# Optimization experiments

Measured on AMD Instinct MI355X. Metric: run time of the kernel, lower is better.

## Reference

```python
import jax, jax.numpy as jnp
import numpy as np

jax.config.update("jax_enable_x64", True)  # torch uses int64 labels with wrapping arithmetic

N = 100_000   # nodes
E = 3_200_000 # edges
D = 128       # label classes (argmax dim)
NUM_ITERATIONS = 3


def setup_inputs() -> dict:
    key = jax.random.key(0)
    k1, k2 = jax.random.split(key)
    x = jax.random.normal(k1, (N, D), dtype=jnp.float32)
    edge_index = jax.random.randint(k2, (2, E), 0, N, dtype=jnp.int64)
    return {"x": x, "edge_index": edge_index}


def _edge_exponents(row):
    """For each edge e, number of edges AFTER e (in edge order) sharing the same row.

    The torch loop computes neighborhood[r] = neighborhood[r]*31 + labels[c]
    sequentially over edges, i.e. for a row-group with targets c_1..c_k (edge order)
    the result is sum_j labels[c_j] * 31**(k - j). The exponent (k - j) is exactly
    the count of later same-row edges.
    """
    e = row.shape[0]
    order = jnp.argsort(row, stable=True)          # stable sort preserves edge order within groups
    srow = row[order]
    first = jnp.searchsorted(srow, srow, side="left")   # group start index
    last = jnp.searchsorted(srow, srow, side="right")   # group end index (exclusive)
    pos = jnp.arange(e) - first                          # position within group
    exp_sorted = (last - first) - 1 - pos                # edges remaining after this one
    return jnp.zeros(e, dtype=jnp.int64).at[order].set(exp_sorted)


def reference(x, edge_index):
    labels = jnp.argmax(x, axis=-1).astype(jnp.int64) if x.ndim > 1 else x.astype(jnp.int64)
    row, col = edge_index[0], edge_index[1]
    exps = _edge_exponents(row)
    # 31**exp in wrapping int64 arithmetic; exponentiation-by-squaring mod 2^64
    # matches the sequential multiply-add mod 2^64 of the torch loop.
    pow31 = jnp.power(jnp.int64(31), exps)
    history = [labels]
    for _ in range(NUM_ITERATIONS):
        vals = labels[col] * pow31                       # [E] per-edge weighted labels
        labels = jax.ops.segment_sum(vals, row, num_segments=N)  # ordered hash accumulate
        history.append(labels)
    return (labels, *history)
```

## Files before the change

### kernel.cpp

```cpp
#include <hip/hip_runtime.h>
#include <hip/hip_bf16.h>


#define WL_D 128
#define NCH 512
#define GRID_F 2048
#define BT 512
#define MSDW 8
#define BBITS 7
#define BROWS 128
#define NBK 1024
#define RLSHIFT 23
#define COLMASK ((1u << RLSHIFT) - 1u)
#define CMAX 5120
#define NBMAX 13
#define KBMAX 10
#define HP8 2487512833u

__device__ inline int xcd_chunk(int bid) { return ((bid & 7) << 6) | (bid >> 3); }

template <int BITS>
__device__ inline unsigned long long match_key(unsigned v) {
    unsigned long long m = ~0ull;
    #pragma unroll
    for (int b = 0; b < BITS; ++b) {
        unsigned long long s = __ballot((v >> b) & 1u);
        m &= ((v >> b) & 1u) ? s : ~s;
    }
    return m;
}

__global__ void __launch_bounds__(BT)
k_hist_argmax(const float* __restrict__ x, const int* __restrict__ ei,
              unsigned* __restrict__ lab0, unsigned* __restrict__ hist,
              int N, int E, int chunk, int nbuckets) {
    __shared__ unsigned h[NBK];
    int bid = blockIdx.x, t = threadIdx.x, lane = t & 63, w = t >> 6;
    if (bid < NCH) {
        int b = xcd_chunk(bid);
        for (int i = t; i < nbuckets; i += BT) h[i] = 0u;
        __syncthreads();
        int base = b * chunk, lim = min(base + chunk, E);
        int vbeg = (base + 3) & ~3; if (vbeg > lim) vbeg = lim;
        int vend = lim & ~3;        if (vend < vbeg) vend = vbeg;
        for (int e = base + t; e < vbeg; e += BT)
            atomicAdd(&h[((unsigned)ei[e]) >> BBITS], 1u);
        for (int i = vbeg + 4 * t; i < vend; i += 4 * BT) {
            int4 v4 = *(const int4*)(ei + i);
            atomicAdd(&h[((unsigned)v4.x) >> BBITS], 1u);
            atomicAdd(&h[((unsigned)v4.y) >> BBITS], 1u);
            atomicAdd(&h[((unsigned)v4.z) >> BBITS], 1u);
            atomicAdd(&h[((unsigned)v4.w) >> BBITS], 1u);
        }
        for (int e = vend + t; e < lim; e += BT)
            atomicAdd(&h[((unsigned)ei[e]) >> BBITS], 1u);
        __syncthreads();
        for (int v = t; v < nbuckets; v += BT) hist[(size_t)v * NCH + b] = h[v];
    } else {
        int ab = bid - NCH;
        int half = lane >> 5, li = lane & 31;
        for (int pr = ab * MSDW + w; 2 * pr < N; pr += (GRID_F - NCH) * MSDW) {
            int r = 2 * pr + half;
            float bv = -3.4e38f; int bi = 0;
            if (r < N) {
                float4 v = ((const float4*)(x + (size_t)r * WL_D))[li];
                bv = v.x; bi = 4 * li;
                if (v.y > bv) { bv = v.y; bi = 4 * li + 1; }
                if (v.z > bv) { bv = v.z; bi = 4 * li + 2; }
                if (v.w > bv) { bv = v.w; bi = 4 * li + 3; }
            }
            #pragma unroll
            for (int off = 16; off > 0; off >>= 1) {
                float ov = __shfl_down(bv, off, 32);
                int   oi = __shfl_down(bi, off, 32);
                if (ov > bv || (ov == bv && oi < bi)) { bv = ov; bi = oi; }
            }
            if (li == 0 && r < N) lab0[r] = (unsigned)bi;
        }
    }
}

__global__ void __launch_bounds__(BT)
k_scan_tile(unsigned* __restrict__ hist, unsigned* __restrict__ bsums, int L) {
    __shared__ unsigned smem[BT];
    int b = blockIdx.x, t = threadIdx.x;
    int i0 = b * 1024;
    unsigned v0 = (i0 + 2 * t     < L) ? hist[i0 + 2 * t]     : 0u;
    unsigned v1 = (i0 + 2 * t + 1 < L) ? hist[i0 + 2 * t + 1] : 0u;
    unsigned s = v0 + v1;
    smem[t] = s;
    __syncthreads();
    for (int o = 1; o < BT; o <<= 1) {
        unsigned u = (t >= o) ? smem[t - o] : 0u;
        __syncthreads();
        smem[t] += u;
        __syncthreads();
    }
    unsigned excl = smem[t] - s;
    if (i0 + 2 * t     < L) hist[i0 + 2 * t]     = excl;
    if (i0 + 2 * t + 1 < L) hist[i0 + 2 * t + 1] = excl + v0;
    if (t == BT - 1) bsums[b] = smem[BT - 1];
}

__global__ void __launch_bounds__(BT)
k_transp(const unsigned* __restrict__ hist, const unsigned* __restrict__ bsums,
         unsigned* __restrict__ histT, unsigned* __restrict__ bstart,
         int nbuckets, int ntiles, int E) {
    __shared__ unsigned tl[64][65];
    __shared__ unsigned sb[BT];
    int t = threadIdx.x;
    unsigned my = (t < ntiles) ? bsums[t] : 0u;
    sb[t] = my;
    __syncthreads();
    for (int o = 1; o < BT; o <<= 1) {
        unsigned u = (t >= o) ? sb[t - o] : 0u;
        __syncthreads();
        sb[t] += u;
        __syncthreads();
    }
    sb[t] -= my;
    __syncthreads();
    int vtiles = (nbuckets + 63) / 64;
    int bx = blockIdx.x % vtiles;
    int by = blockIdx.x / vtiles;
    int tx = t & 63, ty = t >> 6;
    int vb = bx * 64, b0 = by * 64;
    #pragma unroll
    for (int r = 0; r < 8; ++r) {
        int row = r * 8 + ty;
        int v = vb + row;
        size_t idx = (size_t)v * NCH + (b0 + tx);
        tl[row][tx] = (v < nbuckets) ? (hist[idx] + sb[idx >> 10]) : 0u;
    }
    __syncthreads();
    #pragma unroll
    for (int r = 0; r < 8; ++r) {
        int row = r * 8 + ty;
        int v = vb + tx;
        if (v < nbuckets) histT[(size_t)(b0 + row) * nbuckets + v] = tl[tx][row];
    }
    if (by == 0 && t < 64) {
        int v = vb + t;
        if (v < nbuckets) bstart[v] = tl[t][0];
    }
    if (blockIdx.x == 0 && t == 64) bstart[nbuckets] = (unsigned)E;
}

__global__ void __launch_bounds__(BT, 6)
k_scatter(const int* __restrict__ ei, const unsigned* __restrict__ histT,
          unsigned* __restrict__ buf, int E, int chunk, int nbuckets) {
    __shared__ unsigned wbase[MSDW * NBK];
    int b = xcd_chunk(blockIdx.x);
    int t = threadIdx.x, lane = t & 63, w = t >> 6;
    unsigned long long lmask = (1ull << lane) - 1ull;
    for (int i = t; i < MSDW * NBK; i += BT) wbase[i] = 0u;
    __syncthreads();
    int base = b * chunk, lim = min(base + chunk, E);
    int sub  = (chunk + MSDW - 1) / MSDW;
    int wbeg = base + w * sub;
    int wend = min(wbeg + sub, lim);
    int nbat = (wbeg < wend) ? ((wend - wbeg + 63) >> 6) : 0;
    unsigned r_[NBMAX];
    #pragma unroll
    for (int k = 0; k < NBMAX; ++k) {
        int e = wbeg + k * 64 + lane;
        r_[k] = (e < wend) ? (unsigned)ei[e] : 0u;
    }
    #pragma unroll
    for (int k = 0; k < NBMAX; ++k) {
        if (k >= nbat) break;
        int e = wbeg + k * 64 + lane;
        bool act = (e < wend);
        unsigned v = act ? (r_[k] >> BBITS) : (NBK - 1u);
        unsigned long long m = match_key<10>(v);
        unsigned before = (unsigned)__popcll(m & lmask);
        if (act && before == 0u) wbase[w * NBK + v] += (unsigned)__popcll(m);
    }
    for (int k = NBMAX; k < nbat; ++k) {
        int e = wbeg + k * 64 + lane;
        bool act = (e < wend);
        unsigned v = act ? (((unsigned)ei[e]) >> BBITS) : (NBK - 1u);
        unsigned long long m = match_key<10>(v);
        unsigned before = (unsigned)__popcll(m & lmask);
        if (act && before == 0u) wbase[w * NBK + v] += (unsigned)__popcll(m);
    }
    __syncthreads();
    for (int v = t; v < nbuckets; v += BT) {
        unsigned g = histT[(size_t)b * nbuckets + v];
        #pragma unroll
        for (int w2 = 0; w2 < MSDW; ++w2) {
            unsigned cnt = wbase[w2 * NBK + v];
            wbase[w2 * NBK + v] = g;
            g += cnt;
        }
    }
    __syncthreads();
    unsigned c_[NBMAX];
    #pragma unroll
    for (int k = 0; k < NBMAX; ++k) {
        int e = wbeg + k * 64 + lane;
        c_[k] = (e < wend) ? (unsigned)ei[(size_t)E + e] : 0u;
    }
    #pragma unroll
    for (int k = 0; k < NBMAX; ++k) {
        if (k >= nbat) break;
        int e = wbeg + k * 64 + lane;
        bool act = (e < wend);
        unsigned r = r_[k], col = c_[k];
        unsigned v = act ? (r >> BBITS) : (NBK - 1u);
        unsigned long long m = match_key<10>(v);
        unsigned before = (unsigned)__popcll(m & lmask);
        int leader = __ffsll(m) - 1;
        unsigned base0 = 0;
        if (act && before == 0u) {
            base0 = wbase[w * NBK + v];
            wbase[w * NBK + v] = base0 + (unsigned)__popcll(m);
        }
        base0 = __shfl(base0, leader, 64);
        if (act) buf[base0 + before] = ((r & (BROWS - 1u)) << RLSHIFT) | col;
    }
    for (int k = NBMAX; k < nbat; ++k) {
        int e = wbeg + k * 64 + lane;
        bool act = (e < wend);
        unsigned r   = act ? (unsigned)ei[e] : 0u;
        unsigned col = act ? (unsigned)ei[(size_t)E + e] : 0u;
        unsigned v = act ? (r >> BBITS) : (NBK - 1u);
        unsigned long long m = match_key<10>(v);
        unsigned before = (unsigned)__popcll(m & lmask);
        unsigned total  = (unsigned)__popcll(m);
        int leader = __ffsll(m) - 1;
        unsigned base0 = 0;
        if (act && before == 0u) { base0 = wbase[w * NBK + v]; wbase[w * NBK + v] = base0 + total; }
        base0 = __shfl(base0, leader, 64);
        if (act) buf[base0 + before] = ((r & (BROWS - 1u)) << RLSHIFT) | col;
    }
}

__global__ void __launch_bounds__(BT)
k_bucket(const unsigned* __restrict__ buf, const unsigned* __restrict__ bstart,
         unsigned* __restrict__ csr, unsigned* __restrict__ rs_g,
         const unsigned* __restrict__ lab0, unsigned* __restrict__ lab1,
         int N, int E, int nbuckets) {
    __shared__ unsigned data2[CMAX];
    __shared__ unsigned h2[MSDW * BROWS];
    __shared__ unsigned offs[BROWS];
    int bb = blockIdx.x, t = threadIdx.x, lane = t & 63, w = t >> 6;
    unsigned long long lmask = (1ull << lane) - 1ull;
    unsigned start = bstart[bb];
    unsigned end   = bstart[bb + 1];
    unsigned len = end - start;
    bool lds_ok = (len <= CMAX);
    for (int i = t; i < MSDW * BROWS; i += BT) h2[i] = 0u;
    __syncthreads();
    unsigned sub  = (len + MSDW - 1u) / MSDW;
    unsigned wbeg = w * sub;
    unsigned wend = min(wbeg + sub, len);
    int nbat = (wbeg < wend) ? (int)((wend - wbeg + 63u) >> 6) : 0;
    unsigned d_[KBMAX];
    #pragma unroll
    for (int k = 0; k < KBMAX; ++k) {
        unsigned i = wbeg + (unsigned)(k * 64 + lane);
        d_[k] = (i < wend) ? buf[start + i] : 0u;
    }
    #pragma unroll
    for (int k = 0; k < KBMAX; ++k) {
        if (k >= nbat) break;
        unsigned i = wbeg + (unsigned)(k * 64 + lane);
        bool act = (i < wend);
        unsigned v = act ? (d_[k] >> RLSHIFT) : 255u;
        unsigned long long m = match_key<8>(v);
        unsigned before = (unsigned)__popcll(m & lmask);
        unsigned total  = (unsigned)__popcll(m);
        if (act && before == 0u) h2[w * BROWS + v] += total;
    }
    for (int k = KBMAX; k < nbat; ++k) {
        unsigned i = wbeg + (unsigned)(k * 64 + lane);
        bool act = (i < wend);
        unsigned v = act ? (buf[start + i] >> RLSHIFT) : 255u;
        unsigned long long m = match_key<8>(v);
        unsigned before = (unsigned)__popcll(m & lmask);
        unsigned total  = (unsigned)__popcll(m);
        if (act && before == 0u) h2[w * BROWS + v] += total;
    }
    __syncthreads();
    unsigned hv = 0;
    if (t < BROWS) {
        #pragma unroll
        for (int w2 = 0; w2 < MSDW; ++w2) hv += h2[w2 * BROWS + t];
        offs[t] = hv;
    }
    __syncthreads();
    if (t < 64) {
        unsigned a = offs[t], b2 = offs[t + 64];
        #pragma unroll
        for (int o = 1; o < 64; o <<= 1) {
            unsigned ua = __shfl_up(a, o, 64);
            unsigned ub = __shfl_up(b2, o, 64);
            if (t >= o) { a += ua; b2 += ub; }
        }
        unsigned tot = __shfl(a, 63, 64);
        offs[t] = a;
        offs[t + 64] = b2 + tot;
    }
    __syncthreads();
    if (t < BROWS) {
        unsigned excl = offs[t] - hv;
        int row = bb * BROWS + t;
        if (row < N) rs_g[row] = start + excl;
        unsigned g = lds_ok ? excl : (start + excl);
        #pragma unroll
        for (int w2 = 0; w2 < MSDW; ++w2) {
            unsigned cnt = h2[w2 * BROWS + t];
            h2[w2 * BROWS + t] = g;
            g += cnt;
        }
    }
    __syncthreads();
    #pragma unroll
    for (int k = 0; k < KBMAX; ++k) {
        if (k >= nbat) break;
        unsigned i = wbeg + (unsigned)(k * 64 + lane);
        bool act = (i < wend);
        unsigned p = d_[k];
        unsigned v = act ? (p >> RLSHIFT) : 255u;
        unsigned long long m = match_key<8>(v);
        unsigned before = (unsigned)__popcll(m & lmask);
        unsigned total  = (unsigned)__popcll(m);
        int leader = __ffsll(m) - 1;
        unsigned base0 = 0;
        if (act && before == 0u) { base0 = h2[w * BROWS + v]; h2[w * BROWS + v] = base0 + total; }
        base0 = __shfl(base0, leader, 64);
        if (act) {
            if (lds_ok) data2[base0 + before] = p & COLMASK;
            else        csr[base0 + before]   = p & COLMASK;
        }
    }
    for (int k = KBMAX; k < nbat; ++k) {
        unsigned i = wbeg + (unsigned)(k * 64 + lane);
        bool act = (i < wend);
        unsigned p = act ? buf[start + i] : 0u;
        unsigned v = act ? (p >> RLSHIFT) : 255u;
        unsigned long long m = match_key<8>(v);
        unsigned before = (unsigned)__popcll(m & lmask);
        unsigned total  = (unsigned)__popcll(m);
        int leader = __ffsll(m) - 1;
        unsigned base0 = 0;
        if (act && before == 0u) { base0 = h2[w * BROWS + v]; h2[w * BROWS + v] = base0 + total; }
        base0 = __shfl(base0, leader, 64);
        if (act) {
            if (lds_ok) data2[base0 + before] = p & COLMASK;
            else        csr[base0 + before]   = p & COLMASK;
        }
    }
    __syncthreads();
    if (lds_ok) for (unsigned i = t; i < len; i += BT) csr[start + i] = data2[i];
    const unsigned H1 = HP8, H2 = HP8 * HP8, H3 = H2 * HP8, H4 = H3 * HP8;
    const unsigned* srcp = lds_ok ? (const unsigned*)data2 : (csr + start);
    int l = t & 7;
    for (int r0 = t >> 3; r0 < BROWS; r0 += BT / 8) {
        unsigned beg = r0 ? offs[r0 - 1] : 0u;
        unsigned d   = offs[r0] - beg;
        unsigned h = 0u;
        unsigned M = (d > (unsigned)l) ? ((d - (unsigned)l + 7u) >> 3) : 0u;
        unsigned bidx = beg + (unsigned)l;
        unsigned m = 0;
        for (; m + 4u <= M; m += 4u) {
            unsigned c0 = srcp[bidx + 8u * m];
            unsigned c1 = srcp[bidx + 8u * m + 8u];
            unsigned c2 = srcp[bidx + 8u * m + 16u];
            unsigned c3 = srcp[bidx + 8u * m + 24u];
            unsigned l0 = lab0[c0], l1 = lab0[c1], l2 = lab0[c2], l3 = lab0[c3];
            h = h * H4 + l0 * H3 + l1 * H2 + l2 * H1 + l3;
        }
        for (; m + 2u <= M; m += 2u) {
            unsigned c0 = srcp[bidx + 8u * m];
            unsigned c1 = srcp[bidx + 8u * m + 8u];
            h = h * H2 + lab0[c0] * H1 + lab0[c1];
        }
        for (; m < M; ++m) h = h * H1 + lab0[srcp[bidx + 8u * m]];
        if (M) {
            unsigned T = d - 1u - (unsigned)l - 8u * (M - 1u);
            unsigned p = ((T & 1u) ? 31u : 1u) * ((T & 2u) ? 961u : 1u)
                       * ((T & 4u) ? 923521u : 1u);
            h *= p;
        }
        h += __shfl_xor(h, 1, 64);
        h += __shfl_xor(h, 2, 64);
        h += __shfl_xor(h, 4, 64);
        int row = bb * BROWS + r0;
        if (l == 0 && row < N) lab1[row] = h;
    }
}

__device__ inline unsigned horner8(const unsigned* __restrict__ csr,
                                   const unsigned* __restrict__ rs,
                                   const unsigned* __restrict__ lin,
                                   int g, int l, int N, int E) {
    const unsigned H1 = HP8, H2 = HP8 * HP8, H3 = H2 * HP8, H4 = H3 * HP8;
    unsigned s = rs[g];
    unsigned e = (g + 1 < N) ? rs[g + 1] : (unsigned)E;
    unsigned d = e - s;
    unsigned h = 0u;
    unsigned M = (d > (unsigned)l) ? ((d - (unsigned)l + 7u) >> 3) : 0u;
    unsigned bidx = s + (unsigned)l;
    unsigned m = 0;
    for (; m + 4u <= M; m += 4u) {
        unsigned c0 = csr[bidx + 8u * m];
        unsigned c1 = csr[bidx + 8u * m + 8u];
        unsigned c2 = csr[bidx + 8u * m + 16u];
        unsigned c3 = csr[bidx + 8u * m + 24u];
        unsigned l0 = lin[c0], l1 = lin[c1], l2 = lin[c2], l3 = lin[c3];
        h = h * H4 + l0 * H3 + l1 * H2 + l2 * H1 + l3;
    }
    for (; m + 2u <= M; m += 2u) {
        unsigned c0 = csr[bidx + 8u * m];
        unsigned c1 = csr[bidx + 8u * m + 8u];
        h = h * H2 + lin[c0] * H1 + lin[c1];
    }
    for (; m < M; ++m) h = h * H1 + lin[csr[bidx + 8u * m]];
    if (M) {
        unsigned T = d - 1u - (unsigned)l - 8u * (M - 1u);
        unsigned p = ((T & 1u) ? 31u : 1u) * ((T & 2u) ? 961u : 1u)
                   * ((T & 4u) ? 923521u : 1u);
        h *= p;
    }
    h += __shfl_xor(h, 1, 64);
    h += __shfl_xor(h, 2, 64);
    h += __shfl_xor(h, 4, 64);
    return h;
}

__global__ void __launch_bounds__(BT)
k_prop(const unsigned* __restrict__ csr, const unsigned* __restrict__ rs,
       const unsigned* __restrict__ lin, unsigned* __restrict__ lout,
       int N, int E) {
    int idx = blockIdx.x * BT + threadIdx.x;
    int g = idx >> 3, l = idx & 7;
    if (g >= N) return;
    unsigned h = horner8(csr, rs, lin, g, l, N, E);
    if (l == 0) lout[g] = h;
}

__global__ void __launch_bounds__(BT)
k_prop_final(const unsigned* __restrict__ csr, const unsigned* __restrict__ rs,
             const unsigned* __restrict__ lin, const unsigned* __restrict__ l0,
             const unsigned* __restrict__ l1, int* __restrict__ out,
             int N, int E, int pgrid) {
    int idx = blockIdx.x * BT + threadIdx.x;
    int g = idx >> 3, l = idx & 7;
    if (g < N) {
        unsigned h = horner8(csr, rs, lin, g, l, N, E);
        if (l == 0) { out[g] = (int)h; out[4 * N + g] = (int)h; }
    }
    for (int i = idx; i < N; i += pgrid * BT) {
        out[N + i]     = (int)l0[i];
        out[2 * N + i] = (int)l1[i];
        out[3 * N + i] = (int)lin[i];
    }
}

extern "C" void kernel_launch(void* const* d_in, const int* in_sizes, int n_in,
                              void* d_out, int out_size, void* d_ws, size_t ws_size,
                              hipStream_t stream) {
    const float* x  = (const float*)d_in[0];
    const int*   ei = (const int*)d_in[1];
    int* out = (int*)d_out;

    int N = in_sizes[0] / WL_D;
    int E = in_sizes[1] / 2;
    int chunk    = (E + NCH - 1) / NCH;
    int nbuckets = (N + BROWS - 1) / BROWS;
    int L        = nbuckets * NCH;
    int ntiles   = (L + 1023) / 1024;
    int vtiles   = (nbuckets + 63) / 64;
    int btiles   = NCH / 64;
    int pgrid    = (8 * N + BT - 1) / BT;

    unsigned* ws    = (unsigned*)d_ws;
    unsigned* lab0  = ws;
    unsigned* lab1  = lab0 + N;
    unsigned* lab2  = lab1 + N;
    unsigned* rs    = lab2 + N;
    unsigned* bs    = rs + N;
    unsigned* bstart= bs + 1024;
    unsigned* hist  = bstart + 1024;
    unsigned* buf   = hist + L;
    unsigned* csr   = buf + E;
    unsigned* histT = csr;

    k_hist_argmax<<<GRID_F, BT, 0, stream>>>(x, ei, lab0, hist, N, E, chunk, nbuckets);
    k_scan_tile<<<ntiles, BT, 0, stream>>>(hist, bs, L);
    k_transp<<<vtiles * btiles, BT, 0, stream>>>(hist, bs, histT, bstart, nbuckets, ntiles, E);
    k_scatter<<<NCH, BT, 0, stream>>>(ei, histT, buf, E, chunk, nbuckets);
    k_bucket<<<nbuckets, BT, 0, stream>>>(buf, bstart, csr, rs, lab0, lab1, N, E, nbuckets);
    k_prop<<<pgrid, BT, 0, stream>>>(csr, rs, lab1, lab2, N, E);
    k_prop_final<<<pgrid, BT, 0, stream>>>(csr, rs, lab2, lab0, lab1, out, N, E, pgrid);
}
```

Baseline: 197.7 us.

## Replace tile scan and transpose with per-bucket totals and wave-level scan

The two-stage block scan plus tiled transpose of the bucket-by-chunk histogram is replaced by two kernels. One computes per-bucket totals with a wave reduction. The other has each wave sum the totals of all earlier buckets for its offset, scan its bucket's 512 chunk counts with wave shuffles, and write the transposed exclusive offsets through shared memory. This removes the barrier-heavy LDS scan loops and restructures the prefix computation. In exchange, each wave redundantly sums up to ~780 earlier totals, and the transposed stores write only 8 consecutive words per chunk row.

```diff
diff --git a/kernel.cpp b/kernel.cpp
--- a/kernel.cpp
+++ b/kernel.cpp
@@ -81,69 +81,54 @@
 }
 
 __global__ void __launch_bounds__(BT)
-k_scan_tile(unsigned* __restrict__ hist, unsigned* __restrict__ bsums, int L) {
-    __shared__ unsigned smem[BT];
-    int b = blockIdx.x, t = threadIdx.x;
-    int i0 = b * 1024;
-    unsigned v0 = (i0 + 2 * t     < L) ? hist[i0 + 2 * t]     : 0u;
-    unsigned v1 = (i0 + 2 * t + 1 < L) ? hist[i0 + 2 * t + 1] : 0u;
-    unsigned s = v0 + v1;
-    smem[t] = s;
-    __syncthreads();
-    for (int o = 1; o < BT; o <<= 1) {
-        unsigned u = (t >= o) ? smem[t - o] : 0u;
-        __syncthreads();
-        smem[t] += u;
-        __syncthreads();
-    }
-    unsigned excl = smem[t] - s;
-    if (i0 + 2 * t     < L) hist[i0 + 2 * t]     = excl;
-    if (i0 + 2 * t + 1 < L) hist[i0 + 2 * t + 1] = excl + v0;
-    if (t == BT - 1) bsums[b] = smem[BT - 1];
-}
-
-__global__ void __launch_bounds__(BT)
-k_transp(const unsigned* __restrict__ hist, const unsigned* __restrict__ bsums,
-         unsigned* __restrict__ histT, unsigned* __restrict__ bstart,
-         int nbuckets, int ntiles, int E) {
-    __shared__ unsigned tl[64][65];
-    __shared__ unsigned sb[BT];
-    int t = threadIdx.x;
-    unsigned my = (t < ntiles) ? bsums[t] : 0u;
-    sb[t] = my;
-    __syncthreads();
-    for (int o = 1; o < BT; o <<= 1) {
-        unsigned u = (t >= o) ? sb[t - o] : 0u;
-        __syncthreads();
-        sb[t] += u;
-        __syncthreads();
-    }
-    sb[t] -= my;
-    __syncthreads();
-    int vtiles = (nbuckets + 63) / 64;
-    int bx = blockIdx.x % vtiles;
-    int by = blockIdx.x / vtiles;
-    int tx = t & 63, ty = t >> 6;
-    int vb = bx * 64, b0 = by * 64;
-    #pragma unroll
-    for (int r = 0; r < 8; ++r) {
-        int row = r * 8 + ty;
-        int v = vb + row;
-        size_t idx = (size_t)v * NCH + (b0 + tx);
-        tl[row][tx] = (v < nbuckets) ? (hist[idx] + sb[idx >> 10]) : 0u;
-    }
-    __syncthreads();
-    #pragma unroll
-    for (int r = 0; r < 8; ++r) {
-        int row = r * 8 + ty;
-        int v = vb + tx;
-        if (v < nbuckets) histT[(size_t)(b0 + row) * nbuckets + v] = tl[tx][row];
-    }
-    if (by == 0 && t < 64) {
-        int v = vb + t;
-        if (v < nbuckets) bstart[v] = tl[t][0];
-    }
-    if (blockIdx.x == 0 && t == 64) bstart[nbuckets] = (unsigned)E;
+k_btot(const unsigned* __restrict__ hist, unsigned* __restrict__ btot,
+       int nbuckets) {
+    int t = threadIdx.x, w = t >> 6, lane = t & 63;
+    int v = blockIdx.x * MSDW + w;
+    if (v >= nbuckets) return;
+    unsigned s = 0;
+    #pragma unroll
+    for (int j = 0; j < NCH / 64; ++j) s += hist[(size_t)v * NCH + j * 64 + lane];
+    #pragma unroll
+    for (int o = 1; o < 64; o <<= 1) s += __shfl_xor(s, o, 64);
+    if (lane == 0) btot[v] = s;
+}
+
+__global__ void __launch_bounds__(BT)
+k_prep(const unsigned* __restrict__ hist, const unsigned* __restrict__ btot,
+       unsigned* __restrict__ histT, unsigned* __restrict__ bstart,
+       int nbuckets, int E) {
+    __shared__ unsigned tile[NCH * 9];
+    __shared__ unsigned sS[MSDW];
+    int t = threadIdx.x, w = t >> 6, lane = t & 63;
+    int v = blockIdx.x * MSDW + w;
+    bool act = (v < nbuckets);
+    unsigned S = 0;
+    if (act) for (int u = lane; u < v; u += 64) S += btot[u];
+    #pragma unroll
+    for (int o = 1; o < 64; o <<= 1) S += __shfl_xor(S, o, 64);
+    if (lane == 0) { sS[w] = act ? S : 0u; if (act) bstart[v] = S; }
+    if (blockIdx.x == 0 && t == 0) bstart[nbuckets] = (unsigned)E;
+    unsigned carry = 0;
+    #pragma unroll
+    for (int j = 0; j < NCH / 64; ++j) {
+        unsigned xv = act ? hist[(size_t)v * NCH + j * 64 + lane] : 0u;
+        unsigned a = xv;
+        #pragma unroll
+        for (int o = 1; o < 64; o <<= 1) {
+            unsigned u = __shfl_up(a, o, 64);
+            if (lane >= o) a += u;
+        }
+        unsigned excl = a - xv + carry;
+        carry += __shfl(a, 63, 64);
+        tile[(j * 64 + lane) * 9 + w] = excl;
+    }
+    __syncthreads();
+    for (int i = t; i < NCH * MSDW; i += BT) {
+        int c = i >> 3, w2 = i & 7;
+        int v2 = blockIdx.x * MSDW + w2;
+        if (v2 < nbuckets) histT[(size_t)c * nbuckets + v2] = tile[c * 9 + w2] + sS[w2];
+    }
 }
 
 __global__ void __launch_bounds__(BT, 6)
@@ -471,9 +456,7 @@
     int chunk    = (E + NCH - 1) / NCH;
     int nbuckets = (N + BROWS - 1) / BROWS;
     int L        = nbuckets * NCH;
-    int ntiles   = (L + 1023) / 1024;
-    int vtiles   = (nbuckets + 63) / 64;
-    int btiles   = NCH / 64;
+    int pbk      = (nbuckets + MSDW - 1) / MSDW;
     int pgrid    = (8 * N + BT - 1) / BT;
 
     unsigned* ws    = (unsigned*)d_ws;
@@ -481,16 +464,16 @@
     unsigned* lab1  = lab0 + N;
     unsigned* lab2  = lab1 + N;
     unsigned* rs    = lab2 + N;
-    unsigned* bs    = rs + N;
-    unsigned* bstart= bs + 1024;
+    unsigned* btot  = rs + N;
+    unsigned* bstart= btot + 1024;
     unsigned* hist  = bstart + 1024;
     unsigned* buf   = hist + L;
     unsigned* csr   = buf + E;
     unsigned* histT = csr;
 
     k_hist_argmax<<<GRID_F, BT, 0, stream>>>(x, ei, lab0, hist, N, E, chunk, nbuckets);
-    k_scan_tile<<<ntiles, BT, 0, stream>>>(hist, bs, L);
-    k_transp<<<vtiles * btiles, BT, 0, stream>>>(hist, bs, histT, bstart, nbuckets, ntiles, E);
+    k_btot<<<pbk, BT, 0, stream>>>(hist, btot, nbuckets);
+    k_prep<<<pbk, BT, 0, stream>>>(hist, btot, histT, bstart, nbuckets, E);
     k_scatter<<<NCH, BT, 0, stream>>>(ei, histT, buf, E, chunk, nbuckets);
     k_bucket<<<nbuckets, BT, 0, stream>>>(buf, bstart, csr, rs, lab0, lab1, N, E, nbuckets);
     k_prop<<<pgrid, BT, 0, stream>>>(csr, rs, lab1, lab2, N, E);
```

Measured after the change: 196.5 us, median of 2. No clear change (-0.6%).
